# Performance work log

Hardware: AMD Instinct MI355X
Metric: run time of the kernel (lower is better)

Reference implementation:

```python
import jax, jax.numpy as jnp
import numpy as np

DIM = 768
HEADS = 12
HEAD_DIM = DIM // HEADS
SCALE = HEAD_DIM ** -0.5


def setup_inputs() -> dict:
    key = jax.random.key(0)
    k1, k2, k3, k4, k5 = jax.random.split(key, 5)
    x = jax.random.normal(k1, (8, 1024, DIM), dtype=jnp.float32)
    # torch Linear default init ~ U(-1/sqrt(fan_in), 1/sqrt(fan_in)); scale similarly
    s = 1.0 / np.sqrt(DIM)
    qkv_w = jax.random.uniform(k2, (3 * DIM, DIM), minval=-s, maxval=s, dtype=jnp.float32)
    qkv_b = jax.random.uniform(k3, (3 * DIM,), minval=-s, maxval=s, dtype=jnp.float32)
    proj_w = jax.random.uniform(k4, (DIM, DIM), minval=-s, maxval=s, dtype=jnp.float32)
    proj_b = jax.random.uniform(k5, (DIM,), minval=-s, maxval=s, dtype=jnp.float32)
    return {"x": x, "qkv_w": qkv_w, "qkv_b": qkv_b, "proj_w": proj_w, "proj_b": proj_b}


def reference(x, qkv_w, qkv_b, proj_w, proj_b):
    B, N, C = x.shape
    qkv = x @ qkv_w.T + qkv_b                      # [B, N, 3C]
    qkv = qkv.reshape(B, N, 3, HEADS, HEAD_DIM)
    q = jnp.transpose(qkv[:, :, 0], (0, 2, 1, 3))  # [B, H, N, D]
    k = jnp.transpose(qkv[:, :, 1], (0, 2, 1, 3))
    v = jnp.transpose(qkv[:, :, 2], (0, 2, 1, 3))
    attn = jnp.einsum('bhnd,bhmd->bhnm', q, k) * SCALE  # [B, H, N, N]
    attn = jax.nn.softmax(attn, axis=-1)
    out = jnp.einsum('bhnm,bhmd->bhnd', attn, v)   # [B, H, N, D]
    out = jnp.transpose(out, (0, 2, 1, 3)).reshape(B, N, C)
    return out @ proj_w.T + proj_b
```

## Files before the change

### kernel.cpp

```cpp
#include <hip/hip_runtime.h>
#include <stdint.h>

typedef unsigned short ushort_t;
typedef __attribute__((ext_vector_type(8))) short short8;
typedef __attribute__((ext_vector_type(4))) float f32x4;
typedef __attribute__((address_space(1))) uint32_t as1_u32;
typedef __attribute__((address_space(3))) uint32_t as3_u32;

#define MFMA16(a, b, c) __builtin_amdgcn_mfma_f32_16x16x32_bf16(a, b, c, 0, 0, 0)

__device__ __forceinline__ void cp16(const void* g, void* l) {
    __builtin_amdgcn_global_load_lds((as1_u32*)(uintptr_t)g,
                                     (as3_u32*)(uint32_t)(uintptr_t)l, 16, 0, 0);
}

__device__ __forceinline__ ushort_t f2bf(float f) {
    uint32_t u = __float_as_uint(f);
    u += 0x7fffu + ((u >> 16) & 1u);
    return (ushort_t)(u >> 16);
}


__global__ __launch_bounds__(256) void cvt3_kernel(const float* __restrict__ x,
                                                   const float* __restrict__ w1,
                                                   const float* __restrict__ w2,
                                                   ushort_t* __restrict__ xb,
                                                   ushort_t* __restrict__ wb1,
                                                   ushort_t* __restrict__ wb2) {
    const int bid = blockIdx.x;
    const float4* src;
    ushort_t* dst;
    int i;
    if (bid < 6144)      { src = (const float4*)x;  dst = xb;  i = bid * 256 + threadIdx.x; }
    else if (bid < 7872) { src = (const float4*)w1; dst = wb1; i = (bid - 6144) * 256 + threadIdx.x; }
    else                 { src = (const float4*)w2; dst = wb2; i = (bid - 7872) * 256 + threadIdx.x; }
    float4 v = src[i];
    ushort4 o;
    o.x = f2bf(v.x); o.y = f2bf(v.y); o.z = f2bf(v.z); o.w = f2bf(v.w);
    const int e0 = i * 4;
    const int r = e0 / 768, k0 = e0 - r * 768;
    const int off = (((r >> 4) * 24 + (k0 >> 5)) << 9) +
                    (((r & 15) + (((k0 & 31) >> 3) << 4)) << 3) + (k0 & 7);
    *(ushort4*)&dst[off] = o;
}

__global__ __launch_bounds__(256) void qkv_gemm(const ushort_t* __restrict__ xp,
                                                const ushort_t* __restrict__ wqp,
                                                const float* __restrict__ bias,
                                                ushort_t* __restrict__ Qg,
                                                ushort_t* __restrict__ Kg,
                                                ushort_t* __restrict__ Vt) {
    __shared__ __align__(16) ushort_t smem[9216];
    const int t = threadIdx.x, w = t >> 6, lane = t & 63;
    const int m16 = lane & 15, q = lane >> 4;
    const int wgid = blockIdx.x;
    const int xcd = wgid & 7, idx = wgid >> 3;
    const int n0 = (idx % 36) * 64;
    const int m0 = (xcd * 8 + idx / 36) * 128;

    const int rA = (m0 >> 4) + w * 2;
    const int rB = n0 >> 4;
    const int le = lane << 3;

    f32x4 acc[2][4];
#pragma unroll
    for (int i = 0; i < 2; ++i)
#pragma unroll
        for (int j = 0; j < 4; ++j) acc[i][j] = (f32x4)0.f;

#pragma unroll 4
    for (int kki = 0; kki < 24; ++kki) {
        short8 a[2], b[4];
#pragma unroll
        for (int i = 0; i < 2; ++i)
            a[i] = *(const short8*)&xp[(((rA + i) * 24 + kki) << 9) + le];
#pragma unroll
        for (int j = 0; j < 4; ++j)
            b[j] = *(const short8*)&wqp[(((rB + j) * 24 + kki) << 9) + le];
#pragma unroll
        for (int i = 0; i < 2; ++i)
#pragma unroll
            for (int j = 0; j < 4; ++j) acc[i][j] = MFMA16(a[i], b[j], acc[i][j]);
    }

    const int three = n0 / 768;
    const int b_idx = m0 >> 10;
    const int col0 = n0 - three * 768;
    const int hh = col0 >> 6;

    if (three < 2) {
        ushort_t* dst = three ? Kg : Qg;
        const float scale = three ? 1.0f : 0.18033688011112042f;
#pragma unroll
        for (int j = 0; j < 4; ++j) {
            float bj = bias[n0 + j * 16 + m16];
#pragma unroll
            for (int i = 0; i < 2; ++i)
#pragma unroll
                for (int r = 0; r < 4; ++r)
                    smem[(w * 32 + i * 16 + q * 4 + r) * 72 + j * 16 + m16] =
                        f2bf((acc[i][j][r] + bj) * scale);
        }
        __syncthreads();
#pragma unroll
        for (int u4 = 0; u4 < 4; ++u4) {
            int u = u4 * 256 + t;
            int row = u >> 3, cg = u & 7;
            uint4 vv = *(const uint4*)&smem[row * 72 + cg * 8];
            int n = (m0 & 1023) + row;
            *(uint4*)&dst[((b_idx * 12 + hh) * 1024 + n) * 64 + cg * 8] = vv;
        }
    } else {
        const int nq_base = (m0 & 1023) + w * 32;
#pragma unroll
        for (int j = 0; j < 4; ++j) {
            int dd = j * 16 + m16;
            float bj = bias[1536 + col0 + dd];
            ushort_t* base = Vt + ((b_idx * 12 + hh) * 64 + dd) * 1024;
#pragma unroll
            for (int i = 0; i < 2; ++i) {
                ushort4 pk;
                pk.x = f2bf(acc[i][j][0] + bj);
                pk.y = f2bf(acc[i][j][1] + bj);
                pk.z = f2bf(acc[i][j][2] + bj);
                pk.w = f2bf(acc[i][j][3] + bj);
                *(ushort4*)&base[nq_base + i * 16 + q * 4] = pk;
            }
        }
    }
}

__global__ __launch_bounds__(256) void attn_kernel(const ushort_t* __restrict__ Qg,
                                                   const ushort_t* __restrict__ Kg,
                                                   const ushort_t* __restrict__ Vt,
                                                   ushort_t* __restrict__ Ogp) {
    __shared__ __align__(16) ushort_t Ks[64 * 64];
    __shared__ __align__(16) ushort_t Vs[64 * 64];
    __shared__ __align__(16) ushort_t Ps[4 * 16 * 72];
    const int t = threadIdx.x, w = t >> 6, lane = t & 63;
    const int m16 = lane & 15, q = lane >> 4;
    const int wgid = blockIdx.x;
    const int xcd = wgid & 7, idx = wgid >> 3;
    const int bh = xcd * 12 + (idx >> 4);
    const int qt = idx & 15;
    const int b = bh / 12, h = bh % 12;
    const ushort_t* Qbh = Qg + bh * 65536;
    const ushort_t* Kbh = Kg + bh * 65536;
    const ushort_t* Vbh = Vt + bh * 65536;
    ushort_t* Pw = &Ps[w * 1152];

    const int q0 = qt * 64 + w * 16;
    short8 qf[2];
#pragma unroll
    for (int kd = 0; kd < 2; ++kd)
        qf[kd] = *(const short8*)&Qbh[(q0 + m16) * 64 + kd * 32 + q * 8];

    f32x4 o[4];
#pragma unroll
    for (int ds = 0; ds < 4; ++ds) o[ds] = (f32x4)0.f;
    float l_run = 0.f;

    for (int kt = 0; kt < 16; ++kt) {
        const int key0 = kt * 64;
#pragma unroll
        for (int p = 0; p < 2; ++p) {
            const int c = p * 256 + t;
            const int lbase = (p * 256 + w * 64) * 8;
            { int key = c >> 3, g = c & 7;
              cp16(&Kbh[(key0 + key) * 64 + ((g ^ (key & 7)) * 8)], &Ks[lbase]); }
            { int d = c >> 3, g2 = c & 7;
              cp16(&Vbh[d * 1024 + key0 + ((g2 ^ (d & 7)) * 8)], &Vs[lbase]); }
        }
        __syncthreads();

        f32x4 st[4];
#pragma unroll
        for (int ks = 0; ks < 4; ++ks) {
            const ushort_t* kr = &Ks[(ks * 16 + m16) * 64];
            short8 a0 = *(const short8*)&kr[(q ^ (m16 & 7)) * 8];
            short8 a1 = *(const short8*)&kr[((4 + q) ^ (m16 & 7)) * 8];
            st[ks] = MFMA16(a1, qf[1], MFMA16(a0, qf[0], (f32x4)0.f));
        }

        float ps = 0.f;
#pragma unroll
        for (int ks = 0; ks < 4; ++ks) {
            float p0 = exp2f(st[ks][0]);
            float p1 = exp2f(st[ks][1]);
            float p2 = exp2f(st[ks][2]);
            float p3 = exp2f(st[ks][3]);
            ps += (p0 + p1) + (p2 + p3);
            uint32_t u0 = __float_as_uint(p0) + 0x8000u;
            uint32_t u1 = __float_as_uint(p1) + 0x8000u;
            uint32_t u2 = __float_as_uint(p2) + 0x8000u;
            uint32_t u3 = __float_as_uint(p3) + 0x8000u;
            uint2 pk;
            pk.x = __builtin_amdgcn_perm(u1, u0, 0x07060302u);
            pk.y = __builtin_amdgcn_perm(u3, u2, 0x07060302u);
            *(uint2*)&Pw[m16 * 72 + ks * 16 + q * 4] = pk;
        }
        ps += __shfl_xor(ps, 16, 64);
        ps += __shfl_xor(ps, 32, 64);
        l_run += ps;
#pragma unroll
        for (int kkk = 0; kkk < 2; ++kkk) {
            short8 ap = *(const short8*)&Pw[m16 * 72 + kkk * 32 + q * 8];
#pragma unroll
            for (int ds = 0; ds < 4; ++ds) {
                short8 vb = *(const short8*)&Vs[(ds * 16 + m16) * 64 + (((kkk * 4 + q) ^ (m16 & 7)) * 8)];
                o[ds] = MFMA16(ap, vb, o[ds]);
            }
        }
        __syncthreads();
    }
    {
        const int rt = (b * 64 + qt * 4 + w) * 24 + h * 2;
        float linv = 1.f / l_run;
#pragma unroll
        for (int r = 0; r < 4; ++r) {
            float lr = __shfl(linv, q * 4 + r, 64);
#pragma unroll
            for (int ds = 0; ds < 4; ++ds) {
                int off = ((rt + (ds >> 1)) << 9) +
                          ((q * 4 + r + (((ds & 1) << 1) + (m16 >> 3)) * 16) << 3) + (m16 & 7);
                Ogp[off] = f2bf(o[ds][r] * lr);
            }
        }
    }
}

__global__ __launch_bounds__(256) void proj_gemm(const ushort_t* __restrict__ Ogp,
                                                 const ushort_t* __restrict__ wpp,
                                                 const float* __restrict__ bias,
                                                 float* __restrict__ out) {
    const int t = threadIdx.x, w = t >> 6, lane = t & 63;
    const int m16 = lane & 15, q = lane >> 4;
    const int wgid = blockIdx.x;
    const int xcd = wgid & 7, idx = wgid >> 3;
    const int n0 = (idx % 12) * 64;
    const int m0 = (xcd * 8 + idx / 12) * 128;

    const int rA = (m0 >> 4) + w * 2;
    const int rB = n0 >> 4;
    const int le = lane << 3;

    f32x4 acc[2][4];
#pragma unroll
    for (int i = 0; i < 2; ++i)
#pragma unroll
        for (int j = 0; j < 4; ++j) acc[i][j] = (f32x4)0.f;

#pragma unroll 4
    for (int kki = 0; kki < 24; ++kki) {
        short8 a[2], b[4];
#pragma unroll
        for (int i = 0; i < 2; ++i)
            a[i] = *(const short8*)&Ogp[(((rA + i) * 24 + kki) << 9) + le];
#pragma unroll
        for (int j = 0; j < 4; ++j)
            b[j] = *(const short8*)&wpp[(((rB + j) * 24 + kki) << 9) + le];
#pragma unroll
        for (int i = 0; i < 2; ++i)
#pragma unroll
            for (int j = 0; j < 4; ++j) acc[i][j] = MFMA16(a[i], b[j], acc[i][j]);
    }

#pragma unroll
    for (int j = 0; j < 4; ++j) {
        int col = n0 + j * 16 + m16;
        float bj = bias[col];
#pragma unroll
        for (int i = 0; i < 2; ++i)
#pragma unroll
            for (int r = 0; r < 4; ++r) {
                int row = m0 + w * 32 + i * 16 + q * 4 + r;
                out[row * 768 + col] = acc[i][j][r] + bj;
            }
    }
}

extern "C" void kernel_launch(void* const* d_in, const int* in_sizes, int n_in,
                              void* d_out, int out_size, void* d_ws, size_t ws_size,
                              hipStream_t stream) {
    const float* x      = (const float*)d_in[0];
    const float* qkv_w  = (const float*)d_in[1];
    const float* qkv_b  = (const float*)d_in[2];
    const float* proj_w = (const float*)d_in[3];
    const float* proj_b = (const float*)d_in[4];
    float* out = (float*)d_out;

    char* ws = (char*)d_ws;
    ushort_t* xb    = (ushort_t*)(ws);
    ushort_t* wqkv  = (ushort_t*)(ws + 12582912);
    ushort_t* wproj = (ushort_t*)(ws + 16121856);
    ushort_t* Qg    = (ushort_t*)(ws + 17301504);
    ushort_t* Kg    = (ushort_t*)(ws + 29884416);
    ushort_t* Vt    = (ushort_t*)(ws + 42467328);
    ushort_t* Og    = (ushort_t*)(ws + 55050240);

    cvt3_kernel<<<8448, 256, 0, stream>>>(x, qkv_w, proj_w, xb, wqkv, wproj);
    qkv_gemm<<<2304, 256, 0, stream>>>(xb, wqkv, qkv_b, Qg, Kg, Vt);
    attn_kernel<<<1536, 256, 0, stream>>>(Qg, Kg, Vt, Og);
    proj_gemm<<<768, 256, 0, stream>>>(Og, wproj, proj_b, out);
}
```

Baseline: 208.8 us.

## Rework conversion indexing, read V directly from global, halve projection GEMM tile

The conversion kernel now has each thread own one packed 8-element destination chunk, so it does one contiguous 16-byte store per thread and half as many blocks. The attention kernel stops staging V in shared memory and reads V fragments straight from global memory inside the PV loop. The projection GEMM drops from 128-row to 64-row tiles, doubling the grid for better occupancy and parallelism. The V change cuts LDS traffic and footprint but adds uncached, less coalesced global reads in the inner loop. The smaller projection tile also reduces reuse of the B operand.

```diff
diff --git a/kernel.cpp b/kernel.cpp
--- a/kernel.cpp
+++ b/kernel.cpp
@@ -27,21 +27,22 @@
                                                    ushort_t* __restrict__ xb,
                                                    ushort_t* __restrict__ wb1,
                                                    ushort_t* __restrict__ wb2) {
-    const int bid = blockIdx.x;
-    const float4* src;
+    int c = blockIdx.x * 256 + threadIdx.x;
+    const float* src;
     ushort_t* dst;
-    int i;
-    if (bid < 6144)      { src = (const float4*)x;  dst = xb;  i = bid * 256 + threadIdx.x; }
-    else if (bid < 7872) { src = (const float4*)w1; dst = wb1; i = (bid - 6144) * 256 + threadIdx.x; }
-    else                 { src = (const float4*)w2; dst = wb2; i = (bid - 7872) * 256 + threadIdx.x; }
-    float4 v = src[i];
-    ushort4 o;
-    o.x = f2bf(v.x); o.y = f2bf(v.y); o.z = f2bf(v.z); o.w = f2bf(v.w);
-    const int e0 = i * 4;
-    const int r = e0 / 768, k0 = e0 - r * 768;
-    const int off = (((r >> 4) * 24 + (k0 >> 5)) << 9) +
-                    (((r & 15) + (((k0 & 31) >> 3) << 4)) << 3) + (k0 & 7);
-    *(ushort4*)&dst[off] = o;
+    if (c < 786432)       { src = x;  dst = xb; }
+    else if (c < 1007616) { src = w1; dst = wb1; c -= 786432; }
+    else                  { src = w2; dst = wb2; c -= 1007616; }
+    const int tile = c >> 6, inner = c & 63;
+    const int rt = tile / 24, kt = tile - rt * 24;
+    const int r = rt * 16 + (inner & 15);
+    const int k = kt * 32 + ((inner >> 4) << 3);
+    const float4* s4 = (const float4*)&src[r * 768 + k];
+    float4 v0 = s4[0], v1 = s4[1];
+    ushort_t o[8];
+    o[0] = f2bf(v0.x); o[1] = f2bf(v0.y); o[2] = f2bf(v0.z); o[3] = f2bf(v0.w);
+    o[4] = f2bf(v1.x); o[5] = f2bf(v1.y); o[6] = f2bf(v1.z); o[7] = f2bf(v1.w);
+    *(uint4*)&dst[c << 3] = *(const uint4*)o;
 }
 
 __global__ __launch_bounds__(256) void qkv_gemm(const ushort_t* __restrict__ xp,
@@ -135,7 +136,6 @@
                                                    const ushort_t* __restrict__ Vt,
                                                    ushort_t* __restrict__ Ogp) {
     __shared__ __align__(16) ushort_t Ks[64 * 64];
-    __shared__ __align__(16) ushort_t Vs[64 * 64];
     __shared__ __align__(16) ushort_t Ps[4 * 16 * 72];
     const int t = threadIdx.x, w = t >> 6, lane = t & 63;
     const int m16 = lane & 15, q = lane >> 4;
@@ -165,11 +165,8 @@
 #pragma unroll
         for (int p = 0; p < 2; ++p) {
             const int c = p * 256 + t;
-            const int lbase = (p * 256 + w * 64) * 8;
-            { int key = c >> 3, g = c & 7;
-              cp16(&Kbh[(key0 + key) * 64 + ((g ^ (key & 7)) * 8)], &Ks[lbase]); }
-            { int d = c >> 3, g2 = c & 7;
-              cp16(&Vbh[d * 1024 + key0 + ((g2 ^ (d & 7)) * 8)], &Vs[lbase]); }
+            int key = c >> 3, g = c & 7;
+            cp16(&Kbh[(key0 + key) * 64 + ((g ^ (key & 7)) * 8)], &Ks[(p * 256 + w * 64) * 8]);
         }
         __syncthreads();
 
@@ -207,7 +204,7 @@
             short8 ap = *(const short8*)&Pw[m16 * 72 + kkk * 32 + q * 8];
 #pragma unroll
             for (int ds = 0; ds < 4; ++ds) {
-                short8 vb = *(const short8*)&Vs[(ds * 16 + m16) * 64 + (((kkk * 4 + q) ^ (m16 & 7)) * 8)];
+                short8 vb = *(const short8*)&Vbh[(ds * 16 + m16) * 1024 + key0 + (kkk * 4 + q) * 8];
                 o[ds] = MFMA16(ap, vb, o[ds]);
             }
         }
@@ -238,31 +235,25 @@
     const int wgid = blockIdx.x;
     const int xcd = wgid & 7, idx = wgid >> 3;
     const int n0 = (idx % 12) * 64;
-    const int m0 = (xcd * 8 + idx / 12) * 128;
-
-    const int rA = (m0 >> 4) + w * 2;
+    const int m0 = (xcd * 16 + idx / 12) * 64;
+
+    const int rA = (m0 >> 4) + w;
     const int rB = n0 >> 4;
     const int le = lane << 3;
 
-    f32x4 acc[2][4];
-#pragma unroll
-    for (int i = 0; i < 2; ++i)
-#pragma unroll
-        for (int j = 0; j < 4; ++j) acc[i][j] = (f32x4)0.f;
+    f32x4 acc[4];
+#pragma unroll
+    for (int j = 0; j < 4; ++j) acc[j] = (f32x4)0.f;
 
 #pragma unroll 4
     for (int kki = 0; kki < 24; ++kki) {
-        short8 a[2], b[4];
-#pragma unroll
-        for (int i = 0; i < 2; ++i)
-            a[i] = *(const short8*)&Ogp[(((rA + i) * 24 + kki) << 9) + le];
+        short8 a = *(const short8*)&Ogp[((rA * 24 + kki) << 9) + le];
+        short8 b[4];
 #pragma unroll
         for (int j = 0; j < 4; ++j)
             b[j] = *(const short8*)&wpp[(((rB + j) * 24 + kki) << 9) + le];
 #pragma unroll
-        for (int i = 0; i < 2; ++i)
-#pragma unroll
-            for (int j = 0; j < 4; ++j) acc[i][j] = MFMA16(a[i], b[j], acc[i][j]);
+        for (int j = 0; j < 4; ++j) acc[j] = MFMA16(a, b[j], acc[j]);
     }
 
 #pragma unroll
@@ -270,12 +261,10 @@
         int col = n0 + j * 16 + m16;
         float bj = bias[col];
 #pragma unroll
-        for (int i = 0; i < 2; ++i)
-#pragma unroll
-            for (int r = 0; r < 4; ++r) {
-                int row = m0 + w * 32 + i * 16 + q * 4 + r;
-                out[row * 768 + col] = acc[i][j][r] + bj;
-            }
+        for (int r = 0; r < 4; ++r) {
+            int row = m0 + w * 16 + q * 4 + r;
+            out[row * 768 + col] = acc[j][r] + bj;
+        }
     }
 }
 
@@ -298,8 +287,8 @@
     ushort_t* Vt    = (ushort_t*)(ws + 42467328);
     ushort_t* Og    = (ushort_t*)(ws + 55050240);
 
-    cvt3_kernel<<<8448, 256, 0, stream>>>(x, qkv_w, proj_w, xb, wqkv, wproj);
+    cvt3_kernel<<<4224, 256, 0, stream>>>(x, qkv_w, proj_w, xb, wqkv, wproj);
     qkv_gemm<<<2304, 256, 0, stream>>>(xb, wqkv, qkv_b, Qg, Kg, Vt);
     attn_kernel<<<1536, 256, 0, stream>>>(Qg, Kg, Vt, Og);
-    proj_gemm<<<768, 256, 0, stream>>>(Og, wproj, proj_b, out);
-}
+    proj_gemm<<<1536, 256, 0, stream>>>(Og, wproj, proj_b, out);
+}
```

Result: slower. 267.4 us (+28.1%).
